# Optimization experiments

Hardware: AMD Instinct MI355X
Metric: run time of the kernel (lower is better)

## Reference

```python
import jax, jax.numpy as jnp
import numpy as np

N_NODES = 50000
N_EDGES = 600000
D = 128
APPNP_K = 5
APPNP_ALPHA = 0.2


def _mish(x):
    return x * jnp.tanh(jax.nn.softplus(x))


def setup_inputs() -> dict:
    key = jax.random.key(0)
    ks = jax.random.split(key, 6)
    x = jax.random.normal(ks[0], (N_NODES, D), dtype=jnp.float32)
    src = jax.random.randint(ks[1], (N_EDGES,), 0, N_NODES, dtype=jnp.int32)
    dst = jax.random.randint(ks[2], (N_EDGES,), 0, N_NODES, dtype=jnp.int32)
    W1 = jax.random.normal(ks[3], (D, D), dtype=jnp.float32) * (1.0 / np.sqrt(D))
    b1 = jnp.zeros((D,), dtype=jnp.float32)
    W2 = jax.random.normal(ks[4], (2 * D, D), dtype=jnp.float32) * (1.0 / np.sqrt(2 * D))
    b2 = jnp.zeros((D,), dtype=jnp.float32)
    eps1 = jnp.zeros((1,), dtype=jnp.float32)
    eps2 = jnp.zeros((1,), dtype=jnp.float32)
    return {"x": x, "src": src, "dst": dst, "W1": W1, "b1": b1,
            "W2": W2, "b2": b2, "eps1": eps1, "eps2": eps2}


def _appnp(x0, src, dst):
    # DGL APPNPConv: symmetric degree normalization, k power-iteration steps.
    ones = jnp.ones((src.shape[0],), dtype=x0.dtype)
    deg_out = jnp.clip(jax.ops.segment_sum(ones, src, num_segments=N_NODES), 1.0)
    deg_in = jnp.clip(jax.ops.segment_sum(ones, dst, num_segments=N_NODES), 1.0)
    norm_o = deg_out[:, None] ** -0.5  # [N,1]
    norm_i = deg_in[:, None] ** -0.5
    h = x0
    for _ in range(APPNP_K):
        h = h * norm_o
        h = jax.ops.segment_sum(h[src], dst, num_segments=N_NODES)  # gather-scatter
        h = h * norm_i
        h = (1.0 - APPNP_ALPHA) * h + APPNP_ALPHA * x0
    return h


def _gin(h, src, dst, eps, W, b):
    # GINConv(sum, learn_eps): (1+eps)*h + sum_{j in N(i)} h_j, then Linear.
    agg = jax.ops.segment_sum(h[src], dst, num_segments=N_NODES)
    return ((1.0 + eps) * h + agg) @ W + b


def reference(x, src, dst, W1, b1, W2, b2, eps1, eps2):
    out = jnp.tanh(x)           # GCNNorm affects edge weights only; node feats then tanh
    x0 = out                    # res_out[0]
    out = _appnp(out, src, dst)
    out = _gin(out, src, dst, eps1[0], W1, b1)          # layer 0
    out = jnp.concatenate([out, x0], axis=1)            # residual concat
    out = _gin(out, src, dst, eps2[0], W2, b2)          # layer 1
    return _mish(out)
```

## Files before the change

kernel.cpp:

```cpp
#include <hip/hip_runtime.h>
#include <hip/hip_fp16.h>
#include <math.h>

#define NN 50000
#define NE 600000
#define NT ((NN + 31) / 32)

#define HB 64
#define HBINS 12500

typedef _Float16 half8_t __attribute__((ext_vector_type(8)));
typedef float f32x16 __attribute__((ext_vector_type(16)));
typedef float f32x2 __attribute__((ext_vector_type(2)));

union F2H { float2 f; __half2 h[2]; };

__device__ __forceinline__ float2 fp8_dec(unsigned short u) {
  f32x2 v = __builtin_amdgcn_cvt_pk_f32_fp8((unsigned int)u, false);
  float2 r; r.x = v.x; r.y = v.y; return r;
}
__device__ __forceinline__ unsigned short fp8_enc(float a, float b) {
  return (unsigned short)__builtin_amdgcn_cvt_pk_fp8_f32(a, b, 0u, false);
}


__global__ __launch_bounds__(256) void k_tanh(const float* __restrict__ x,
                                              const float* __restrict__ no,
                                              __half2* __restrict__ x0h,
                                              unsigned int* __restrict__ x0n8) {
  int i = blockIdx.x * 256 + threadIdx.x;
  if (i >= NN * 32) return;
  float4 v = reinterpret_cast<const float4*>(x)[i];
  float t[4];
  float vv[4] = {v.x, v.y, v.z, v.w};
  #pragma unroll
  for (int j = 0; j < 4; ++j) {
    float xc = fminf(fmaxf(vv[j], -9.f), 9.f);
    float E = __expf(2.f * xc);
    t[j] = (E - 1.f) / (E + 1.f);
  }
  float s = no[i >> 5];
  F2H a;
  a.h[0] = __floats2half2_rn(t[0], t[1]);
  a.h[1] = __floats2half2_rn(t[2], t[3]);
  reinterpret_cast<float2*>(x0h)[i] = a.f;
  unsigned int p = __builtin_amdgcn_cvt_pk_fp8_f32(t[0] * s, t[1] * s, 0u, false);
  p = __builtin_amdgcn_cvt_pk_fp8_f32(t[2] * s, t[3] * s, p, true);
  x0n8[i] = p;
}

__global__ __launch_bounds__(256) void k_wt(const float* __restrict__ W1,
                                            const float* __restrict__ W2,
                                            _Float16* __restrict__ w1p,
                                            _Float16* __restrict__ w2p) {
  int i = blockIdx.x * 256 + threadIdx.x;
  if (i < 128 * 128) {
    int k = i >> 7, n = i & 127;
    int nb = n >> 5, r = n & 31, ks = k >> 4, g = (k & 15) >> 3, j = k & 7;
    w1p[(((ks << 2) + nb) * 64 + (g << 5) + r) * 8 + j] = (_Float16)W1[i];
  } else {
    int q = i - 128 * 128;
    if (q < 256 * 128) {
      int k = q >> 7, n = q & 127;
      int nb = n >> 5, r = n & 31, ks = k >> 4, g = (k & 15) >> 3, j = k & 7;
      w2p[(((ks << 2) + nb) * 64 + (g << 5) + r) * 8 + j] = (_Float16)W2[q];
    }
  }
}

__global__ __launch_bounds__(1024) void k_hist(const int* __restrict__ src,
                                               const int* __restrict__ dst,
                                               int* __restrict__ hpart) {
  __shared__ int lh[HBINS];
  #pragma unroll 1
  for (int ph = 0; ph < 8; ++ph) {
    const int* idx = (ph & 4) ? dst : src;
    int base = (ph & 3) * HBINS;
    for (int i = threadIdx.x; i < HBINS; i += 1024) lh[i] = 0;
    __syncthreads();
    for (int e = blockIdx.x * 1024 + threadIdx.x; e < NE; e += HB * 1024) {
      int v = idx[e] - base;
      if ((unsigned)v < (unsigned)HBINS) atomicAdd(&lh[v], 1);
    }
    __syncthreads();
    int* outp = hpart + ((size_t)ph * HB + blockIdx.x) * HBINS;
    for (int i = threadIdx.x; i < HBINS; i += 1024) outp[i] = lh[i];
    __syncthreads();
  }
}

__global__ __launch_bounds__(256) void k_merge(const int* __restrict__ hpart,
                                               int* __restrict__ ci,
                                               float* __restrict__ no,
                                               float* __restrict__ ni) {
  int i = blockIdx.x * 256 + threadIdx.x;
  if (i >= NN) return;
  int r = i / HBINS, bin = i - r * HBINS;
  const int* ps = hpart + ((size_t)(0 + r) * HB) * HBINS + bin;
  const int* pd = hpart + ((size_t)(4 + r) * HB) * HBINS + bin;
  int so = 0, si = 0;
  #pragma unroll 8
  for (int b = 0; b < HB; ++b) {
    so += ps[(size_t)b * HBINS];
    si += pd[(size_t)b * HBINS];
  }
  ci[i] = si;
  no[i] = rsqrtf((float)max(so, 1));
  ni[i] = rsqrtf((float)max(si, 1));
}

__global__ __launch_bounds__(1024) void k_scanA(const int* __restrict__ deg,
                                                int* __restrict__ incl,
                                                int* __restrict__ bsum) {
  int tid = threadIdx.x;
  int gid = blockIdx.x * 1024 + tid;
  int v = (gid < NN) ? deg[gid] : 0;
  int lane = tid & 63;
  #pragma unroll
  for (int o = 1; o < 64; o <<= 1) {
    int n = __shfl_up(v, o);
    if (lane >= o) v += n;
  }
  __shared__ int ws[16];
  int wid = tid >> 6;
  if (lane == 63) ws[wid] = v;
  __syncthreads();
  if (tid < 16) {
    int s = ws[tid];
    #pragma unroll
    for (int o = 1; o < 16; o <<= 1) {
      int n = __shfl_up(s, o);
      if (tid >= o) s += n;
    }
    ws[tid] = s;
  }
  __syncthreads();
  if (wid > 0) v += ws[wid - 1];
  if (gid < NN) incl[gid] = v;
  if (tid == 1023) bsum[blockIdx.x] = v;
}

__global__ __launch_bounds__(64) void k_scanB(const int* __restrict__ bsum,
                                              int* __restrict__ boff, int nb) {
  int t = threadIdx.x;
  int v = (t < nb) ? bsum[t] : 0;
  int orig = v;
  #pragma unroll
  for (int o = 1; o < 64; o <<= 1) {
    int n = __shfl_up(v, o);
    if (t >= o) v += n;
  }
  if (t < nb) boff[t] = v - orig;
}

__global__ __launch_bounds__(256) void k_scanC(const int* __restrict__ incl,
                                               const int* __restrict__ deg,
                                               const int* __restrict__ boff,
                                               int* __restrict__ rp) {
  int i = blockIdx.x * 256 + threadIdx.x;
  if (i < NN) rp[i] = incl[i] - deg[i] + boff[i >> 10];
  if (i == 0) rp[NN] = NE;
}

__global__ __launch_bounds__(256) void k_fill(const int* __restrict__ src,
                                              const int* __restrict__ dst,
                                              const int* __restrict__ rp,
                                              int* __restrict__ fill,
                                              int* __restrict__ colsrc) {
  int e = blockIdx.x * 256 + threadIdx.x;
  if (e < NE) {
    int d = dst[e];
    int pos = rp[d] + atomicAdd(&fill[d], 1);
    colsrc[pos] = src[e];
  }
}

#define GATHER_LOOP(LOADEXPR)                                        \
  for (int base = 0; base < cnt; base += 64) {                      \
    int e = beg + base + lane;                                      \
    int cv = (e < end) ? cs[e] : 0;                                 \
    int m = cnt - base; if (m > 64) m = 64;                         \
    int j = 0;                                                      \
    for (; j + 8 <= m; j += 8) {                                    \
      _Pragma("unroll")                                             \
      for (int u = 0; u < 8; ++u) {                                 \
        int s = __builtin_amdgcn_readlane(cv, j + u);               \
        LOADEXPR;                                                   \
      }                                                             \
    }                                                               \
    if (j + 4 <= m) {                                               \
      _Pragma("unroll")                                             \
      for (int u = 0; u < 4; ++u) {                                 \
        int s = __builtin_amdgcn_readlane(cv, j + u);               \
        LOADEXPR;                                                   \
      }                                                             \
      j += 4;                                                       \
    }                                                               \
    if (j + 2 <= m) {                                               \
      _Pragma("unroll")                                             \
      for (int u = 0; u < 2; ++u) {                                 \
        int s = __builtin_amdgcn_readlane(cv, j + u);               \
        LOADEXPR;                                                   \
      }                                                             \
      j += 2;                                                       \
    }                                                               \
    if (j < m) {                                                    \
      int s = __builtin_amdgcn_readlane(cv, j);                     \
      LOADEXPR;                                                     \
    }                                                               \
  }

template <bool LAST>
__global__ __launch_bounds__(256) void k_appnp8(const unsigned short* __restrict__ h8,
                                                const __half2* __restrict__ x0,
                                                const float* __restrict__ no,
                                                const float* __restrict__ ni,
                                                const int* __restrict__ rp,
                                                const int* __restrict__ cs,
                                                unsigned short* __restrict__ out8,
                                                __half2* __restrict__ out16) {
  int w = (blockIdx.x * 256 + threadIdx.x) >> 6;
  int lane = threadIdx.x & 63;
  if (w >= NN) return;
  const unsigned short* hl = h8 + lane;
  int beg = rp[w], end = rp[w + 1], cnt = end - beg;
  float ax = 0.f, ay = 0.f;
  GATHER_LOOP({
    float2 f = fp8_dec(hl[s * 64]);
    ax += f.x; ay += f.y;
  })
  float wi = 0.8f * ni[w];
  float2 xv = __half22float2(x0[w * 64 + lane]);
  float rx = wi * ax + 0.2f * xv.x;
  float ry = wi * ay + 0.2f * xv.y;
  if (LAST) {
    out16[w * 64 + lane] = __floats2half2_rn(rx, ry);
  } else {
    float sc = no[w];
    out8[w * 64 + lane] = fp8_enc(rx * sc, ry * sc);
  }
}

__device__ inline void store_packed(_Float16* __restrict__ zp, int w, int lane,
                                    float v0, float v1) {
  int t = w >> 5, r = w & 31;
  int ks = lane >> 3, g = (lane >> 2) & 1, j = (lane & 3) * 2;
  size_t addr = (((size_t)t * 8 + ks) * 64 + g * 32 + r) * 8 + j;
  *reinterpret_cast<__half2*>(zp + addr) = __floats2half2_rn(v0, v1);
}

__global__ __launch_bounds__(256) void k_appnp_first(const unsigned short* __restrict__ xs8,
                                                     const __half2* __restrict__ xp,
                                                     const float* __restrict__ epsp,
                                                     const float* __restrict__ no,
                                                     const float* __restrict__ ni,
                                                     const int* __restrict__ rp,
                                                     const int* __restrict__ cs,
                                                     unsigned short* __restrict__ hout8,
                                                     _Float16* __restrict__ zout) {
  int w = (blockIdx.x * 256 + threadIdx.x) >> 6;
  int lane = threadIdx.x & 63;
  if (w >= NN) return;
  const unsigned short* xsl = xs8 + lane;
  const __half2* xpl = xp + lane;
  int beg = rp[w], end = rp[w + 1], cnt = end - beg;
  float ax = 0.f, ay = 0.f, bx = 0.f, by = 0.f;
  GATHER_LOOP({
    float2 f = fp8_dec(xsl[s * 64]);
    float2 g2 = __half22float2(xpl[s * 64]);
    ax += f.x; ay += f.y; bx += g2.x; by += g2.y;
  })
  float2 xv = __half22float2(xp[w * 64 + lane]);
  float wi = 0.8f * ni[w];
  float sc = no[w];
  hout8[w * 64 + lane] = fp8_enc(sc * (wi * ax + 0.2f * xv.x),
                                 sc * (wi * ay + 0.2f * xv.y));
  float e2 = 1.0f + epsp[0];
  store_packed(zout, w, lane, e2 * xv.x + bx, e2 * xv.y + by);
}

__global__ __launch_bounds__(256) void k_gather_z(const __half2* __restrict__ h,
                                                  const float* __restrict__ epsp,
                                                  const int* __restrict__ rp,
                                                  const int* __restrict__ cs,
                                                  _Float16* __restrict__ zout) {
  int w = (blockIdx.x * 256 + threadIdx.x) >> 6;
  int lane = threadIdx.x & 63;
  if (w >= NN) return;
  const __half2* hl = h + lane;
  int beg = rp[w], end = rp[w + 1], cnt = end - beg;
  float ax = 0.f, ay = 0.f;
  GATHER_LOOP({
    float2 f = __half22float2(hl[s * 64]);
    ax += f.x; ay += f.y;
  })
  float e1 = 1.0f + epsp[0];
  float2 hv = __half22float2(h[w * 64 + lane]);
  store_packed(zout, w, lane, e1 * hv.x + ax, e1 * hv.y + ay);
}

template <int KTOT, bool MISH>
__global__ __launch_bounds__(64) void k_mgemm(const _Float16* __restrict__ z0,
                                              const _Float16* __restrict__ z1,
                                              const _Float16* __restrict__ wp,
                                              const float* __restrict__ bias,
                                              float* __restrict__ outf,
                                              __half2* __restrict__ outh) {
  int lane = threadIdx.x;
  int t = blockIdx.x;
  int row0 = t * 32;
  if (row0 >= NN) return;
  int r31 = lane & 31, g = lane >> 5;
  f32x16 acc[4];
  #pragma unroll
  for (int i = 0; i < 4; ++i) acc[i] = (f32x16)(0.0f);
  #pragma unroll 4
  for (int ks = 0; ks < KTOT / 16; ++ks) {
    const _Float16* zp = (KTOT == 256 && ks >= 8) ? z1 : z0;
    int kls = (KTOT == 256) ? (ks & 7) : ks;
    half8_t a = *reinterpret_cast<const half8_t*>(
        zp + (((size_t)t * 8 + kls) * 64 + lane) * 8);
    #pragma unroll
    for (int nb = 0; nb < 4; ++nb) {
      half8_t b = *reinterpret_cast<const half8_t*>(
          wp + (((size_t)ks * 4 + nb) * 64 + lane) * 8);
      acc[nb] = __builtin_amdgcn_mfma_f32_32x32x16_f16(a, b, acc[nb], 0, 0, 0);
    }
  }
  #pragma unroll
  for (int nb = 0; nb < 4; ++nb) {
    float bv = bias[nb * 32 + r31];
    #pragma unroll
    for (int r = 0; r < 16; ++r) {
      int rl = (r & 3) + 8 * (r >> 2) + 4 * g;
      int grow = row0 + rl;
      if (grow < NN) {
        float v = acc[nb][r] + bv;
        if (MISH) {
          float E = __expf(v);
          float q = E * (E + 2.f);
          float mv = v * q / (q + 2.f);
          v = (v > 15.f) ? v : mv;
          outf[(size_t)grow * 128 + nb * 32 + r31] = v;
        } else {
          float u = __shfl_xor(v, 1);
          if (!(lane & 1)) {
            outh[((size_t)grow * 128 + nb * 32 + r31) >> 1] = __floats2half2_rn(v, u);
          }
        }
      }
    }
  }
}

extern "C" void kernel_launch(void* const* d_in, const int* in_sizes, int n_in,
                              void* d_out, int out_size, void* d_ws, size_t ws_size,
                              hipStream_t stream) {
  const float* x = (const float*)d_in[0];
  const int* src = (const int*)d_in[1];
  const int* dst = (const int*)d_in[2];
  const float* W1 = (const float*)d_in[3];
  const float* b1 = (const float*)d_in[4];
  const float* W2 = (const float*)d_in[5];
  const float* b2 = (const float*)d_in[6];
  const float* eps1 = (const float*)d_in[7];
  const float* eps2 = (const float*)d_in[8];
  float* out = (float*)d_out;

  char* ws = (char*)d_ws;
  size_t off = 0;
  auto alloc = [&](size_t bytes) -> void* {
    void* p = ws + off;
    off += (bytes + 255) & ~(size_t)255;
    return p;
  };
  const size_t NDP = (size_t)NT * 4096;
  __half2* x0h = (__half2*)alloc(NDP * 2);
  unsigned short* x0n8 = (unsigned short*)alloc(NDP);
  unsigned short* hA8 = (unsigned short*)alloc(NDP);
  unsigned short* hB8 = (unsigned short*)alloc(NDP);
  __half2* h5 = (__half2*)alloc(NDP * 2);
  __half2* zx = (__half2*)alloc(NDP * 2);
  __half2* z1p = (__half2*)alloc(NDP * 2);
  __half2* g1h = (__half2*)alloc(NDP * 2);
  __half2* zg = (__half2*)alloc(NDP * 2);
  _Float16* w1p = (_Float16*)alloc(128 * 128 * 2);
  _Float16* w2p = (_Float16*)alloc(256 * 128 * 2);
  int* ci = (int*)alloc(NN * 4);
  int* fillc = (int*)alloc(NN * 4);
  float* nrm_o = (float*)alloc(NN * 4);
  float* nrm_i = (float*)alloc(NN * 4);
  int* incl = (int*)alloc(NN * 4);
  int* bsum = (int*)alloc(64 * 4);
  int* boff = (int*)alloc(64 * 4);
  int* rp = (int*)alloc((NN + 1) * 4);
  int* colsrc = (int*)alloc(NE * 4);

  int* hpart = (int*)zx;

  hipMemsetAsync(fillc, 0, NN * 4, stream);

  k_hist<<<HB, 1024, 0, stream>>>(src, dst, hpart);
  k_merge<<<(NN + 255) / 256, 256, 0, stream>>>(hpart, ci, nrm_o, nrm_i);

  const int SB = (NN + 1023) / 1024;
  k_scanA<<<SB, 1024, 0, stream>>>(ci, incl, bsum);
  k_scanB<<<1, 64, 0, stream>>>(bsum, boff, SB);
  k_scanC<<<(NN + 255) / 256, 256, 0, stream>>>(incl, ci, boff, rp);
  const int EB = (NE + 255) / 256;
  k_fill<<<EB, 256, 0, stream>>>(src, dst, rp, fillc, colsrc);

  k_tanh<<<(NN * 32 + 255) / 256, 256, 0, stream>>>(x, nrm_o, x0h,
                                                    (unsigned int*)x0n8);
  k_wt<<<192, 256, 0, stream>>>(W1, W2, w1p, w2p);

  const int GB = (NN * 64 + 255) / 256;
  k_appnp_first<<<GB, 256, 0, stream>>>(x0n8, x0h, eps2, nrm_o, nrm_i, rp, colsrc,
                                        hA8, (_Float16*)zx);
  k_appnp8<false><<<GB, 256, 0, stream>>>(hA8, x0h, nrm_o, nrm_i, rp, colsrc,
                                          hB8, nullptr);
  k_appnp8<false><<<GB, 256, 0, stream>>>(hB8, x0h, nrm_o, nrm_i, rp, colsrc,
                                          hA8, nullptr);
  k_appnp8<false><<<GB, 256, 0, stream>>>(hA8, x0h, nrm_o, nrm_i, rp, colsrc,
                                          hB8, nullptr);
  k_appnp8<true><<<GB, 256, 0, stream>>>(hB8, x0h, nrm_o, nrm_i, rp, colsrc,
                                         nullptr, h5);

  k_gather_z<<<GB, 256, 0, stream>>>(h5, eps1, rp, colsrc, (_Float16*)z1p);

  k_mgemm<128, false><<<NT, 64, 0, stream>>>((const _Float16*)z1p, nullptr, w1p, b1,
                                             nullptr, g1h);
  k_gather_z<<<GB, 256, 0, stream>>>(g1h, eps2, rp, colsrc, (_Float16*)zg);
  k_mgemm<256, true><<<NT, 64, 0, stream>>>((const _Float16*)zg, (const _Float16*)zx,
                                            w2p, b2, out, nullptr);
}
```

Measured before the change: 309.8 us.

## Build CSR with LDS-ranked scatter and merge x0 gather into GIN aggregation

The histogram kernel now records each edge's rank within its per-block shared-memory bin. The merge kernel turns the per-block destination counts into exclusive offsets in place, so CSR column filling can use a plain scatter instead of global atomics, and the memset of the fill counter goes away. The first APPNP step now uses the generic fp8 kernel. The gather of neighbour x0 features (zx) moves into a combined kernel that also builds the first GIN aggregation input, so both share one pass over the edge list. This adds an NE-sized rank buffer and extra reads of the partial histograms during scatter.

New measurement: 299.8 us. -3.2%, faster.

```diff
diff --git a/kernel.cpp b/kernel.cpp
--- a/kernel.cpp
+++ b/kernel.cpp
@@ -70,7 +70,8 @@
 
 __global__ __launch_bounds__(1024) void k_hist(const int* __restrict__ src,
                                                const int* __restrict__ dst,
-                                               int* __restrict__ hpart) {
+                                               int* __restrict__ hpart,
+                                               int* __restrict__ lseq) {
   __shared__ int lh[HBINS];
   #pragma unroll 1
   for (int ph = 0; ph < 8; ++ph) {
@@ -78,9 +79,16 @@
     int base = (ph & 3) * HBINS;
     for (int i = threadIdx.x; i < HBINS; i += 1024) lh[i] = 0;
     __syncthreads();
-    for (int e = blockIdx.x * 1024 + threadIdx.x; e < NE; e += HB * 1024) {
-      int v = idx[e] - base;
-      if ((unsigned)v < (unsigned)HBINS) atomicAdd(&lh[v], 1);
+    if (ph & 4) {
+      for (int e = blockIdx.x * 1024 + threadIdx.x; e < NE; e += HB * 1024) {
+        int v = idx[e] - base;
+        if ((unsigned)v < (unsigned)HBINS) lseq[e] = atomicAdd(&lh[v], 1);
+      }
+    } else {
+      for (int e = blockIdx.x * 1024 + threadIdx.x; e < NE; e += HB * 1024) {
+        int v = idx[e] - base;
+        if ((unsigned)v < (unsigned)HBINS) atomicAdd(&lh[v], 1);
+      }
     }
     __syncthreads();
     int* outp = hpart + ((size_t)ph * HB + blockIdx.x) * HBINS;
@@ -89,7 +97,7 @@
   }
 }
 
-__global__ __launch_bounds__(256) void k_merge(const int* __restrict__ hpart,
+__global__ __launch_bounds__(256) void k_merge(int* __restrict__ hpart,
                                                int* __restrict__ ci,
                                                float* __restrict__ no,
                                                float* __restrict__ ni) {
@@ -97,12 +105,16 @@
   if (i >= NN) return;
   int r = i / HBINS, bin = i - r * HBINS;
   const int* ps = hpart + ((size_t)(0 + r) * HB) * HBINS + bin;
-  const int* pd = hpart + ((size_t)(4 + r) * HB) * HBINS + bin;
+  int* pd = hpart + ((size_t)(4 + r) * HB) * HBINS + bin;
   int so = 0, si = 0;
   #pragma unroll 8
+  for (int b = 0; b < HB; ++b) so += ps[(size_t)b * HBINS];
+  #pragma unroll 8
   for (int b = 0; b < HB; ++b) {
-    so += ps[(size_t)b * HBINS];
-    si += pd[(size_t)b * HBINS];
+    int* p = pd + (size_t)b * HBINS;
+    int t = *p;
+    *p = si;
+    si += t;
   }
   ci[i] = si;
   no[i] = rsqrtf((float)max(so, 1));
@@ -162,17 +174,19 @@
   if (i == 0) rp[NN] = NE;
 }
 
-__global__ __launch_bounds__(256) void k_fill(const int* __restrict__ src,
-                                              const int* __restrict__ dst,
-                                              const int* __restrict__ rp,
-                                              int* __restrict__ fill,
-                                              int* __restrict__ colsrc) {
+__global__ __launch_bounds__(256) void k_scatter(const int* __restrict__ src,
+                                                 const int* __restrict__ dst,
+                                                 const int* __restrict__ lseq,
+                                                 const int* __restrict__ hpart,
+                                                 const int* __restrict__ rp,
+                                                 int* __restrict__ colsrc) {
   int e = blockIdx.x * 256 + threadIdx.x;
-  if (e < NE) {
-    int d = dst[e];
-    int pos = rp[d] + atomicAdd(&fill[d], 1);
-    colsrc[pos] = src[e];
-  }
+  if (e >= NE) return;
+  int d = dst[e];
+  int r = d / HBINS, bin = d - r * HBINS;
+  int b = (e >> 10) & (HB - 1);
+  int ofs = hpart[((size_t)(4 + r) * HB + b) * HBINS + bin];
+  colsrc[rp[d] + ofs + lseq[e]] = src[e];
 }
 
 #define GATHER_LOOP(LOADEXPR)                                        \
@@ -249,34 +263,32 @@
   *reinterpret_cast<__half2*>(zp + addr) = __floats2half2_rn(v0, v1);
 }
 
-__global__ __launch_bounds__(256) void k_appnp_first(const unsigned short* __restrict__ xs8,
-                                                     const __half2* __restrict__ xp,
-                                                     const float* __restrict__ epsp,
-                                                     const float* __restrict__ no,
-                                                     const float* __restrict__ ni,
-                                                     const int* __restrict__ rp,
-                                                     const int* __restrict__ cs,
-                                                     unsigned short* __restrict__ hout8,
-                                                     _Float16* __restrict__ zout) {
+__global__ __launch_bounds__(256) void k_gz2(const __half2* __restrict__ h5,
+                                             const __half2* __restrict__ x0,
+                                             const float* __restrict__ eps1p,
+                                             const float* __restrict__ eps2p,
+                                             const int* __restrict__ rp,
+                                             const int* __restrict__ cs,
+                                             _Float16* __restrict__ z1out,
+                                             _Float16* __restrict__ zxout) {
   int w = (blockIdx.x * 256 + threadIdx.x) >> 6;
   int lane = threadIdx.x & 63;
   if (w >= NN) return;
-  const unsigned short* xsl = xs8 + lane;
-  const __half2* xpl = xp + lane;
+  const __half2* hl = h5 + lane;
+  const __half2* xl = x0 + lane;
   int beg = rp[w], end = rp[w + 1], cnt = end - beg;
   float ax = 0.f, ay = 0.f, bx = 0.f, by = 0.f;
   GATHER_LOOP({
-    float2 f = fp8_dec(xsl[s * 64]);
-    float2 g2 = __half22float2(xpl[s * 64]);
+    float2 f = __half22float2(hl[s * 64]);
+    float2 g2 = __half22float2(xl[s * 64]);
     ax += f.x; ay += f.y; bx += g2.x; by += g2.y;
   })
-  float2 xv = __half22float2(xp[w * 64 + lane]);
-  float wi = 0.8f * ni[w];
-  float sc = no[w];
-  hout8[w * 64 + lane] = fp8_enc(sc * (wi * ax + 0.2f * xv.x),
-                                 sc * (wi * ay + 0.2f * xv.y));
-  float e2 = 1.0f + epsp[0];
-  store_packed(zout, w, lane, e2 * xv.x + bx, e2 * xv.y + by);
+  float e1 = 1.0f + eps1p[0];
+  float e2 = 1.0f + eps2p[0];
+  float2 hv = __half22float2(h5[w * 64 + lane]);
+  float2 xv = __half22float2(x0[w * 64 + lane]);
+  store_packed(z1out, w, lane, e1 * hv.x + ax, e1 * hv.y + ay);
+  store_packed(zxout, w, lane, e2 * xv.x + bx, e2 * xv.y + by);
 }
 
 __global__ __launch_bounds__(256) void k_gather_z(const __half2* __restrict__ h,
@@ -387,20 +399,18 @@
   _Float16* w1p = (_Float16*)alloc(128 * 128 * 2);
   _Float16* w2p = (_Float16*)alloc(256 * 128 * 2);
   int* ci = (int*)alloc(NN * 4);
-  int* fillc = (int*)alloc(NN * 4);
   float* nrm_o = (float*)alloc(NN * 4);
   float* nrm_i = (float*)alloc(NN * 4);
   int* incl = (int*)alloc(NN * 4);
   int* bsum = (int*)alloc(64 * 4);
   int* boff = (int*)alloc(64 * 4);
   int* rp = (int*)alloc((NN + 1) * 4);
+  int* lseq = (int*)alloc(NE * 4);
   int* colsrc = (int*)alloc(NE * 4);
 
   int* hpart = (int*)zx;
 
-  hipMemsetAsync(fillc, 0, NN * 4, stream);
-
-  k_hist<<<HB, 1024, 0, stream>>>(src, dst, hpart);
+  k_hist<<<HB, 1024, 0, stream>>>(src, dst, hpart, lseq);
   k_merge<<<(NN + 255) / 256, 256, 0, stream>>>(hpart, ci, nrm_o, nrm_i);
 
   const int SB = (NN + 1023) / 1024;
@@ -408,15 +418,15 @@
   k_scanB<<<1, 64, 0, stream>>>(bsum, boff, SB);
   k_scanC<<<(NN + 255) / 256, 256, 0, stream>>>(incl, ci, boff, rp);
   const int EB = (NE + 255) / 256;
-  k_fill<<<EB, 256, 0, stream>>>(src, dst, rp, fillc, colsrc);
+  k_scatter<<<EB, 256, 0, stream>>>(src, dst, lseq, hpart, rp, colsrc);
 
   k_tanh<<<(NN * 32 + 255) / 256, 256, 0, stream>>>(x, nrm_o, x0h,
                                                     (unsigned int*)x0n8);
   k_wt<<<192, 256, 0, stream>>>(W1, W2, w1p, w2p);
 
   const int GB = (NN * 64 + 255) / 256;
-  k_appnp_first<<<GB, 256, 0, stream>>>(x0n8, x0h, eps2, nrm_o, nrm_i, rp, colsrc,
-                                        hA8, (_Float16*)zx);
+  k_appnp8<false><<<GB, 256, 0, stream>>>(x0n8, x0h, nrm_o, nrm_i, rp, colsrc,
+                                          hA8, nullptr);
   k_appnp8<false><<<GB, 256, 0, stream>>>(hA8, x0h, nrm_o, nrm_i, rp, colsrc,
                                           hB8, nullptr);
   k_appnp8<false><<<GB, 256, 0, stream>>>(hB8, x0h, nrm_o, nrm_i, rp, colsrc,
@@ -426,7 +436,8 @@
   k_appnp8<true><<<GB, 256, 0, stream>>>(hB8, x0h, nrm_o, nrm_i, rp, colsrc,
                                          nullptr, h5);
 
-  k_gather_z<<<GB, 256, 0, stream>>>(h5, eps1, rp, colsrc, (_Float16*)z1p);
+  k_gz2<<<GB, 256, 0, stream>>>(h5, x0h, eps1, eps2, rp, colsrc,
+                                (_Float16*)z1p, (_Float16*)zx);
 
   k_mgemm<128, false><<<NT, 64, 0, stream>>>((const _Float16*)z1p, nullptr, w1p, b1,
                                              nullptr, g1h);
```
